# Performance work log

Measured on AMD Instinct MI355X. Metric: run time of the kernel, lower is better.

Reference implementation:

```python
import jax, jax.numpy as jnp
import numpy as np

H = 256   # hidden_dim
S = 16    # d_state
B = 2
N = 8192
LN_EPS = 1e-5


def setup_inputs() -> dict:
    key = jax.random.key(0)
    ks = jax.random.split(key, 12)
    std = 1.0 / np.sqrt(H)
    inp = {
        'x': jax.random.normal(ks[0], (B, N, H), dtype=jnp.float32),
        'in_w': jax.random.normal(ks[1], (2 * H, H), dtype=jnp.float32) * std,
        'in_b': jax.random.normal(ks[2], (2 * H,), dtype=jnp.float32) * std,
        'xp_w': jax.random.normal(ks[3], (2 * S + 1, H), dtype=jnp.float32) * std,
        'xp_b': jax.random.normal(ks[4], (2 * S + 1,), dtype=jnp.float32) * std,
        'dt_w': jax.random.normal(ks[5], (H, 1), dtype=jnp.float32),
        'dt_b': jax.random.normal(ks[6], (H,), dtype=jnp.float32),
        'A_log': jnp.log(jnp.broadcast_to(jnp.arange(1, S + 1, dtype=jnp.float32), (H, S))),
        'D': jnp.ones((H,), dtype=jnp.float32),
        'out_w': jax.random.normal(ks[7], (H, H), dtype=jnp.float32) * std,
        'out_b': jax.random.normal(ks[8], (H,), dtype=jnp.float32) * std,
        'ln_g': jnp.ones((H,), dtype=jnp.float32),
        'ln_b': jnp.zeros((H,), dtype=jnp.float32),
    }
    return inp


def reference(x, in_w, in_b, xp_w, xp_b, dt_w, dt_b, A_log, D, out_w, out_b, ln_g, ln_b):
    # x: (B, N, H). Dropout is identity in eval mode.
    residual = x
    xz = jnp.einsum('bnh,kh->bnk', x, in_w) + in_b            # (B,N,2H)
    x_inner, z = xz[..., :H], xz[..., H:]
    x_dbl = jnp.einsum('bnh,kh->bnk', x_inner, xp_w) + xp_b   # (B,N,2S+1)
    dt_raw = x_dbl[..., :1]
    B_raw = x_dbl[..., 1:S + 1]                               # (B,N,S)
    C_raw = x_dbl[..., S + 1:]                                # (B,N,S)
    dt = jax.nn.softplus(dt_raw * dt_w[:, 0] + dt_b)          # (B,N,H)
    # NOTE: the original computes dA = exp(dt * A) but never uses it; A_log
    # does not affect the output, so we skip materializing dA.
    dB = dt[..., None] * B_raw[:, :, None, :]                 # (B,N,H,S)
    h = jnp.cumsum(x_inner[..., None] * dB, axis=1)           # (B,N,H,S)
    y = jnp.einsum('bnhs,bns->bnh', h, C_raw) + D * x_inner   # (B,N,H)
    y = y * jax.nn.silu(z)
    out = jnp.einsum('bnh,kh->bnk', y, out_w) + out_b
    r = out + residual
    mu = jnp.mean(r, axis=-1, keepdims=True)
    var = jnp.mean((r - mu) ** 2, axis=-1, keepdims=True)
    return ln_g * (r - mu) * jax.lax.rsqrt(var + LN_EPS) + ln_b
```

## Files before the change

### kernel.cpp

```cpp
#include <hip/hip_runtime.h>
#include <hip/hip_bf16.h>


#define HD 256
#define SD 16
#define NSEQ 8192
#define NBATCH 2
#define BN (NBATCH * NSEQ)
#define CHUNK 32
#define NCHUNK (NSEQ / CHUNK)
#define NGRP 16
#define GSZ (NCHUNK / NGRP)
#define LN_EPS 1e-5f

#define NIW (2 * HD * HD)
#define NXP (48 * HD)
#define NOW (HD * HD)

typedef __hip_bfloat16 bf16;
typedef __attribute__((ext_vector_type(8))) short bf16x8;
typedef __attribute__((ext_vector_type(4))) short short4v;
typedef __attribute__((ext_vector_type(4))) float f32x4;

__device__ __forceinline__ float b2f(bf16 v) { return __bfloat162float(v); }
__device__ __forceinline__ short f2bs(float f) {
  union { bf16 b; short s; } u;
  u.b = __float2bfloat16(f);
  return u.s;
}
__device__ __forceinline__ bf16x8 cvt_frag(const float* p) {
  bf16x8 r;
#pragma unroll
  for (int j = 0; j < 8; ++j) r[j] = f2bs(p[j]);
  return r;
}
__device__ __forceinline__ float softplus_f(float a) {
  return (a > 20.f) ? a : __logf(1.f + __expf(a));
}

__global__ __launch_bounds__(256) void k0_weights(
    const float* __restrict__ in_w, const float* __restrict__ xp_w,
    const float* __restrict__ out_w, bf16* __restrict__ wbin,
    bf16* __restrict__ wbxp, bf16* __restrict__ wbout)
{
  const int base = (blockIdx.x * 256 + threadIdx.x) * 4;
  if (base < NIW) {
    f32x4 v = *(const f32x4*)(in_w + base);
    *(short4v*)((short*)wbin + base) =
        short4v{f2bs(v[0]), f2bs(v[1]), f2bs(v[2]), f2bs(v[3])};
  } else if (base < NIW + NXP) {
    const int off = base - NIW;
    short4v s;
    if (off < 33 * HD) {
      f32x4 v = *(const f32x4*)(xp_w + off);
      s = short4v{f2bs(v[0]), f2bs(v[1]), f2bs(v[2]), f2bs(v[3])};
    } else {
      s = short4v{0, 0, 0, 0};
    }
    *(short4v*)((short*)wbxp + off) = s;
  } else if (base < NIW + NXP + NOW) {
    const int off = base - NIW - NXP;
    f32x4 v = *(const f32x4*)(out_w + off);
    *(short4v*)((short*)wbout + off) =
        short4v{f2bs(v[0]), f2bs(v[1]), f2bs(v[2]), f2bs(v[3])};
  }
}

__global__ __launch_bounds__(512) void k1f_in_xp_sum(
    const float* __restrict__ x, const bf16* __restrict__ wbin,
    const float* __restrict__ in_b, const bf16* __restrict__ wbxp,
    const float* __restrict__ xp_b, const float* __restrict__ dt_w,
    const float* __restrict__ dt_b, bf16* __restrict__ xib,
    bf16* __restrict__ zb, float* __restrict__ dbc, float* __restrict__ Mc)
{
  __shared__ float xt[32][260];
  __shared__ float zt[32][260];
  __shared__ float sdbc[32][33];
  const int tid = threadIdx.x;
  const int wave = tid >> 6, lane = tid & 63, q = lane >> 4, l16 = lane & 15;
  const int R0 = blockIdx.x * CHUNK;

  {
    const int row = tid >> 4;
    const int c0 = (tid & 15) * 16;
    const float* src = x + (size_t)(R0 + row) * HD + c0;
#pragma unroll
    for (int j = 0; j < 4; ++j)
      *(f32x4*)&xt[row][c0 + j * 4] = *(const f32x4*)(src + j * 4);
  }
  __syncthreads();

  const int mrow = (wave & 1) * 16;
  const int colBase = (wave >> 1) * 128;
  f32x4 acc[8] = {};
  {
    const bf16* bp = wbin + (size_t)(colBase + l16) * HD + q * 8;
#pragma unroll
    for (int k = 0; k < HD; k += 32) {
      bf16x8 af = cvt_frag(&xt[mrow + l16][k + q * 8]);
#pragma unroll
      for (int t = 0; t < 8; ++t) {
        bf16x8 bfr = *(const bf16x8*)(bp + (size_t)t * 16 * HD + k);
        acc[t] = __builtin_amdgcn_mfma_f32_16x16x32_bf16(af, bfr, acc[t], 0, 0, 0);
      }
    }
  }
  __syncthreads();

  {
    float (*dst)[260] = (wave < 4) ? xt : zt;
    const int cb = (wave < 4) ? colBase : (colBase - 256);
#pragma unroll
    for (int t = 0; t < 8; ++t) {
      const int gcol = colBase + t * 16 + l16;
      const float bias = in_b[gcol];
#pragma unroll
      for (int r = 0; r < 4; ++r)
        dst[mrow + q * 4 + r][cb + t * 16 + l16] = acc[t][r] + bias;
    }
  }
  __syncthreads();

  {
    const int row = tid >> 4;
    const int c0 = (tid & 15) * 16;
    bf16* xd = xib + (size_t)(R0 + row) * HD + c0;
    bf16* zd = zb + (size_t)(R0 + row) * HD + c0;
    *(bf16x8*)xd = cvt_frag(&xt[row][c0]);
    *(bf16x8*)(xd + 8) = cvt_frag(&xt[row][c0 + 8]);
    *(bf16x8*)zd = cvt_frag(&zt[row][c0]);
    *(bf16x8*)(zd + 8) = cvt_frag(&zt[row][c0 + 8]);
  }

  if (wave < 2) {
    f32x4 pacc[3] = {};
    const bf16* pb = wbxp + (size_t)l16 * HD + q * 8;
#pragma unroll
    for (int k = 0; k < HD; k += 32) {
      bf16x8 af = cvt_frag(&xt[wave * 16 + l16][k + q * 8]);
#pragma unroll
      for (int t = 0; t < 3; ++t) {
        bf16x8 bfr = *(const bf16x8*)(pb + (size_t)t * 16 * HD + k);
        pacc[t] = __builtin_amdgcn_mfma_f32_16x16x32_bf16(af, bfr, pacc[t], 0, 0, 0);
      }
    }
#pragma unroll
    for (int t = 0; t < 3; ++t) {
      const int col = t * 16 + l16;
      if (col < 33) {
        const float bias = xp_b[col];
#pragma unroll
        for (int r = 0; r < 4; ++r)
          sdbc[wave * 16 + q * 4 + r][col] = pacc[t][r] + bias;
      }
    }
  }
  __syncthreads();

  {
    const float* sflat = &sdbc[0][0];
    for (int idx = tid; idx < CHUNK * 33; idx += 512)
      dbc[(size_t)R0 * 33 + idx] = sflat[idx];
  }
  {
    const int h = tid & 255;
    const int sh = tid >> 8;
    const float dtw = dt_w[h], dtb = dt_b[h];
    float st[8] = {};
#pragma unroll
    for (int n = 0; n < CHUNK; ++n) {
      const float xv = xt[n][h];
      const float dt = softplus_f(sdbc[n][0] * dtw + dtb);
      const float u = xv * dt;
#pragma unroll
      for (int s = 0; s < 8; ++s) st[s] += u * sdbc[n][1 + sh * 8 + s];
    }
    const int b = R0 >> 13, c = (R0 & (NSEQ - 1)) >> 5;
    float* mp = Mc + ((size_t)(b * NCHUNK + c)) * 4096 + (sh * 8) * HD + h;
#pragma unroll
    for (int s = 0; s < 8; ++s) mp[s * HD] = st[s];
  }
}

__global__ __launch_bounds__(256) void k4a_prefix_local(
    float* __restrict__ Mc, float* __restrict__ Gs)
{
  const int tid = blockIdx.x * 256 + threadIdx.x;
  const int b = tid >> 16;
  const int g = (tid >> 12) & (NGRP - 1);
  const int hs = tid & 4095;
  float run = 0.f;
#pragma unroll
  for (int i = 0; i < GSZ; ++i) {
    const size_t idx = ((size_t)(b * NCHUNK + g * GSZ + i)) * 4096 + hs;
    const float v = Mc[idx];
    Mc[idx] = run;
    run += v;
  }
  Gs[((size_t)(b * NGRP + g)) * 4096 + hs] = run;
}

__global__ __launch_bounds__(256) void k4b_prefix_groups(float* __restrict__ Gs)
{
  const int tid = blockIdx.x * 256 + threadIdx.x;
  const int b = tid >> 12;
  const int hs = tid & 4095;
  float run = 0.f;
#pragma unroll
  for (int g = 0; g < NGRP; ++g) {
    const size_t idx = ((size_t)(b * NGRP + g)) * 4096 + hs;
    const float v = Gs[idx];
    Gs[idx] = run;
    run += v;
  }
}

__global__ __launch_bounds__(512) void k56_scan_out_ln(
    const bf16* __restrict__ xib, const bf16* __restrict__ zb,
    const float* __restrict__ dbc, const float* __restrict__ dt_w,
    const float* __restrict__ dt_b, const float* __restrict__ Dv,
    const float* __restrict__ Mc, const float* __restrict__ Gs,
    const bf16* __restrict__ wbout, const float* __restrict__ out_b,
    const float* __restrict__ x, const float* __restrict__ ln_g,
    const float* __restrict__ ln_b, float* __restrict__ out)
{
  __shared__ float sdbc[CHUNK][33];
  __shared__ float yt[32][260];
  __shared__ float pt[32][260];
  const int tid = threadIdx.x;
  const int wave = tid >> 6, lane = tid & 63, q = lane >> 4, l16 = lane & 15;
  const int R0 = blockIdx.x * CHUNK;
  const int b = R0 >> 13;
  const int cchunk = (R0 & (NSEQ - 1)) >> 5;

  for (int idx = tid; idx < CHUNK * 33; idx += 512) {
    const int n = idx / 33, j = idx - n * 33;
    sdbc[n][j] = dbc[(size_t)(R0 + n) * 33 + j];
  }
  __syncthreads();

  {
    const int h = tid & 255;
    const int sh = tid >> 8;
    const float dtw = dt_w[h], dtb = dt_b[h];
    const float dv = Dv[h];
    float st[8];
    const float* mp = Mc + ((size_t)(b * NCHUNK + cchunk)) * 4096 + sh * 8 * HD + h;
    const float* gp = Gs + ((size_t)(b * NGRP + cchunk / GSZ)) * 4096 + sh * 8 * HD + h;
#pragma unroll
    for (int s = 0; s < 8; ++s) st[s] = mp[s * HD] + gp[s * HD];
    float (*dst)[260] = (sh == 0) ? yt : pt;
    for (int n = 0; n < CHUNK; ++n) {
      const float xv = b2f(xib[(size_t)(R0 + n) * HD + h]);
      const float dt = softplus_f(sdbc[n][0] * dtw + dtb);
      const float u = xv * dt;
      float y = (sh == 0) ? dv * xv : 0.f;
#pragma unroll
      for (int s = 0; s < 8; ++s) {
        st[s] += u * sdbc[n][1 + sh * 8 + s];
        y += st[s] * sdbc[n][17 + sh * 8 + s];
      }
      dst[n][h] = y;
    }
  }
  __syncthreads();

  {
    const int h = tid & 255;
    const int r2 = tid >> 8;
#pragma unroll
    for (int j = 0; j < 16; ++j) {
      const int row = r2 * 16 + j;
      const float zv = b2f(zb[(size_t)(R0 + row) * HD + h]);
      const float sig = 1.f / (1.f + __expf(-zv));
      yt[row][h] = (yt[row][h] + pt[row][h]) * zv * sig;
    }
  }
  __syncthreads();

  const int mrow = (wave & 1) * 16;
  const int colBase = (wave >> 1) * 64;
  f32x4 acc[4] = {};
  {
    const bf16* bp = wbout + (size_t)(colBase + l16) * HD + q * 8;
#pragma unroll
    for (int k = 0; k < HD; k += 32) {
      bf16x8 af = cvt_frag(&yt[mrow + l16][k + q * 8]);
#pragma unroll
      for (int t = 0; t < 4; ++t) {
        bf16x8 bfr = *(const bf16x8*)(bp + (size_t)t * 16 * HD + k);
        acc[t] = __builtin_amdgcn_mfma_f32_16x16x32_bf16(af, bfr, acc[t], 0, 0, 0);
      }
    }
  }
  __syncthreads();

#pragma unroll
  for (int t = 0; t < 4; ++t) {
    const int col = colBase + t * 16 + l16;
    const float bias = out_b[col];
#pragma unroll
    for (int r = 0; r < 4; ++r) {
      const int row = mrow + q * 4 + r;
      pt[row][col] = acc[t][r] + bias + x[(size_t)(R0 + row) * HD + col];
    }
  }
  __syncthreads();

#pragma unroll
  for (int rr = 0; rr < 4; ++rr) {
    const int row = wave * 4 + rr;
    float p = 0.f;
#pragma unroll
    for (int j = 0; j < 4; ++j) p += pt[row][lane + 64 * j];
#pragma unroll
    for (int off = 32; off > 0; off >>= 1) p += __shfl_xor(p, off);
    const float mu = p * (1.f / 256.f);
    float v2 = 0.f;
#pragma unroll
    for (int j = 0; j < 4; ++j) {
      const float d = pt[row][lane + 64 * j] - mu;
      v2 += d * d;
    }
#pragma unroll
    for (int off = 32; off > 0; off >>= 1) v2 += __shfl_xor(v2, off);
    const float rstd = rsqrtf(v2 * (1.f / 256.f) + LN_EPS);
    const size_t base = (size_t)(R0 + row) * HD;
#pragma unroll
    for (int j = 0; j < 4; ++j) {
      const int cc = lane + 64 * j;
      out[base + cc] = ln_g[cc] * (pt[row][cc] - mu) * rstd + ln_b[cc];
    }
  }
}

extern "C" void kernel_launch(void* const* d_in, const int* in_sizes, int n_in,
                              void* d_out, int out_size, void* d_ws, size_t ws_size,
                              hipStream_t stream)
{
  const float* x     = (const float*)d_in[0];
  const float* in_w  = (const float*)d_in[1];
  const float* in_b  = (const float*)d_in[2];
  const float* xp_w  = (const float*)d_in[3];
  const float* xp_b  = (const float*)d_in[4];
  const float* dt_w  = (const float*)d_in[5];
  const float* dt_b  = (const float*)d_in[6];
  const float* Dv    = (const float*)d_in[8];
  const float* out_w = (const float*)d_in[9];
  const float* out_b = (const float*)d_in[10];
  const float* ln_g  = (const float*)d_in[11];
  const float* ln_b  = (const float*)d_in[12];

  char* ws = (char*)d_ws;
  bf16*  xib   = (bf16*)(ws);
  bf16*  zb    = (bf16*)(ws +  8388608);
  float* dbc   = (float*)(ws + 16777216);
  float* Mc    = (float*)(ws + 18939904);
  float* Gs    = (float*)(ws + 27328512);
  bf16*  wbin  = (bf16*)(ws + 27852800);
  bf16*  wbxp  = (bf16*)(ws + 28114944);
  bf16*  wbout = (bf16*)(ws + 28139520);
  float* out   = (float*)d_out;

  hipLaunchKernelGGL(k0_weights, dim3((NIW + NXP + NOW) / 1024), dim3(256),
                     0, stream, in_w, xp_w, out_w, wbin, wbxp, wbout);
  hipLaunchKernelGGL(k1f_in_xp_sum, dim3(BN / CHUNK), dim3(512), 0, stream,
                     x, wbin, in_b, wbxp, xp_b, dt_w, dt_b,
                     xib, zb, dbc, Mc);
  hipLaunchKernelGGL(k4a_prefix_local, dim3(NBATCH * NGRP * 4096 / 256),
                     dim3(256), 0, stream, Mc, Gs);
  hipLaunchKernelGGL(k4b_prefix_groups, dim3(NBATCH * 4096 / 256), dim3(256),
                     0, stream, Gs);
  hipLaunchKernelGGL(k56_scan_out_ln, dim3(BN / CHUNK), dim3(512), 0, stream,
                     xib, zb, dbc, dt_w, dt_b, Dv, Mc, Gs,
                     wbout, out_b, x, ln_g, ln_b, out);
}
```

Before: 169.5 us.

## Split fused in-projection into tiled GEMM plus separate xp/state-sum kernel

Converts x to bf16 in the prep kernel, then runs the in-projection as a standalone 128x128-tiled MFMA GEMM with the weight tile staged in LDS, replacing the per-32-row fused kernel that re-read all in_w from global for every block. The xp projection and chunk-state summation move to a new 256-thread kernel that stages xi and xp weights in LDS. The out-projection in the final kernel is re-tiled so each wave covers both 16-row halves and reuses each weight fragment twice. It adds a kernel launch plus an extra bf16 round-trip of x and xi through global memory.

Measured after the change: 150.3 us. -11.3%, faster.

```diff
diff --git a/kernel.cpp b/kernel.cpp
--- a/kernel.cpp
+++ b/kernel.cpp
@@ -13,6 +13,7 @@
 #define GSZ (NCHUNK / NGRP)
 #define LN_EPS 1e-5f
 
+#define NX  (BN * HD)
 #define NIW (2 * HD * HD)
 #define NXP (48 * HD)
 #define NOW (HD * HD)
@@ -38,18 +39,24 @@
   return (a > 20.f) ? a : __logf(1.f + __expf(a));
 }
 
-__global__ __launch_bounds__(256) void k0_weights(
-    const float* __restrict__ in_w, const float* __restrict__ xp_w,
-    const float* __restrict__ out_w, bf16* __restrict__ wbin,
+__global__ __launch_bounds__(256) void k0_convert(
+    const float* __restrict__ x, const float* __restrict__ in_w,
+    const float* __restrict__ xp_w, const float* __restrict__ out_w,
+    bf16* __restrict__ xb, bf16* __restrict__ wbin,
     bf16* __restrict__ wbxp, bf16* __restrict__ wbout)
 {
   const int base = (blockIdx.x * 256 + threadIdx.x) * 4;
-  if (base < NIW) {
-    f32x4 v = *(const f32x4*)(in_w + base);
-    *(short4v*)((short*)wbin + base) =
+  if (base < NX) {
+    f32x4 v = *(const f32x4*)(x + base);
+    *(short4v*)((short*)xb + base) =
         short4v{f2bs(v[0]), f2bs(v[1]), f2bs(v[2]), f2bs(v[3])};
-  } else if (base < NIW + NXP) {
-    const int off = base - NIW;
+  } else if (base < NX + NIW) {
+    const int off = base - NX;
+    f32x4 v = *(const f32x4*)(in_w + off);
+    *(short4v*)((short*)wbin + off) =
+        short4v{f2bs(v[0]), f2bs(v[1]), f2bs(v[2]), f2bs(v[3])};
+  } else if (base < NX + NIW + NXP) {
+    const int off = base - NX - NIW;
     short4v s;
     if (off < 33 * HD) {
       f32x4 v = *(const f32x4*)(xp_w + off);
@@ -58,89 +65,116 @@
       s = short4v{0, 0, 0, 0};
     }
     *(short4v*)((short*)wbxp + off) = s;
-  } else if (base < NIW + NXP + NOW) {
-    const int off = base - NIW - NXP;
+  } else if (base < NX + NIW + NXP + NOW) {
+    const int off = base - NX - NIW - NXP;
     f32x4 v = *(const f32x4*)(out_w + off);
     *(short4v*)((short*)wbout + off) =
         short4v{f2bs(v[0]), f2bs(v[1]), f2bs(v[2]), f2bs(v[3])};
   }
 }
 
-__global__ __launch_bounds__(512) void k1f_in_xp_sum(
-    const float* __restrict__ x, const bf16* __restrict__ wbin,
-    const float* __restrict__ in_b, const bf16* __restrict__ wbxp,
+__global__ __launch_bounds__(256) void k1_gemm(
+    const bf16* __restrict__ xb, const bf16* __restrict__ wbin,
+    const float* __restrict__ in_b, bf16* __restrict__ xib,
+    bf16* __restrict__ zb)
+{
+  __shared__ __align__(16) char smem[128 * 264 * 2];
+  bf16* Bt = (bf16*)smem;
+  float* Ct = (float*)smem;
+
+  const int tid = threadIdx.x;
+  const int rt = blockIdx.x >> 2, ct = blockIdx.x & 3;
+  const int R0 = rt * 128, C0 = ct * 128;
+  const int wave = tid >> 6, lane = tid & 63, q = lane >> 4, l16 = lane & 15;
+
+#pragma unroll
+  for (int it = 0; it < 16; ++it) {
+    const int f = tid + it * 256;
+    const int row = f >> 5, g = f & 31;
+    bf16x8 v = *(const bf16x8*)(wbin + (size_t)(C0 + row) * HD + g * 8);
+    *(bf16x8*)(Bt + row * 264 + g * 8) = v;
+  }
+  __syncthreads();
+
+  const int rowHalf = (wave & 1) * 64;
+  const int colHalf = (wave >> 1) * 64;
+  f32x4 acc[4][4] = {};
+  const bf16* ap = xb + (size_t)(R0 + rowHalf + l16) * HD + q * 8;
+#pragma unroll
+  for (int k = 0; k < HD; k += 32) {
+    bf16x8 a[4], b[4];
+#pragma unroll
+    for (int i = 0; i < 4; ++i)
+      a[i] = *(const bf16x8*)(ap + (size_t)i * 16 * HD + k);
+#pragma unroll
+    for (int j = 0; j < 4; ++j)
+      b[j] = *(const bf16x8*)(Bt + (colHalf + j * 16 + l16) * 264 + k + q * 8);
+#pragma unroll
+    for (int i = 0; i < 4; ++i)
+#pragma unroll
+      for (int j = 0; j < 4; ++j)
+        acc[i][j] = __builtin_amdgcn_mfma_f32_16x16x32_bf16(a[i], b[j], acc[i][j], 0, 0, 0);
+  }
+  __syncthreads();
+
+#pragma unroll
+  for (int j = 0; j < 4; ++j) {
+    const int col = colHalf + j * 16 + l16;
+    const float bias = in_b[C0 + col];
+#pragma unroll
+    for (int i = 0; i < 4; ++i)
+#pragma unroll
+      for (int r = 0; r < 4; ++r)
+        Ct[(rowHalf + i * 16 + q * 4 + r) * 132 + col] = acc[i][j][r] + bias;
+  }
+  __syncthreads();
+
+  bf16* dst = (C0 < HD) ? xib : zb;
+  const int Cd = (C0 < HD) ? C0 : (C0 - HD);
+#pragma unroll
+  for (int it = 0; it < 8; ++it) {
+    const int f = tid + it * 256;
+    const int row = f >> 4, g = f & 15;
+    bf16x8 v = cvt_frag(Ct + row * 132 + g * 8);
+    *(bf16x8*)(dst + (size_t)(R0 + row) * HD + Cd + g * 8) = v;
+  }
+}
+
+__global__ __launch_bounds__(256) void k2_xp_sum(
+    const bf16* __restrict__ xib, const bf16* __restrict__ wbxp,
     const float* __restrict__ xp_b, const float* __restrict__ dt_w,
-    const float* __restrict__ dt_b, bf16* __restrict__ xib,
-    bf16* __restrict__ zb, float* __restrict__ dbc, float* __restrict__ Mc)
-{
-  __shared__ float xt[32][260];
-  __shared__ float zt[32][260];
+    const float* __restrict__ dt_b, float* __restrict__ dbc,
+    float* __restrict__ Mc)
+{
+  __shared__ bf16 xt[32 * 264];
+  __shared__ bf16 wp[48 * 264];
   __shared__ float sdbc[32][33];
   const int tid = threadIdx.x;
+  const int R0 = blockIdx.x * CHUNK;
   const int wave = tid >> 6, lane = tid & 63, q = lane >> 4, l16 = lane & 15;
-  const int R0 = blockIdx.x * CHUNK;
-
-  {
-    const int row = tid >> 4;
-    const int c0 = (tid & 15) * 16;
-    const float* src = x + (size_t)(R0 + row) * HD + c0;
-#pragma unroll
-    for (int j = 0; j < 4; ++j)
-      *(f32x4*)&xt[row][c0 + j * 4] = *(const f32x4*)(src + j * 4);
-  }
-  __syncthreads();
-
-  const int mrow = (wave & 1) * 16;
-  const int colBase = (wave >> 1) * 128;
-  f32x4 acc[8] = {};
-  {
-    const bf16* bp = wbin + (size_t)(colBase + l16) * HD + q * 8;
-#pragma unroll
-    for (int k = 0; k < HD; k += 32) {
-      bf16x8 af = cvt_frag(&xt[mrow + l16][k + q * 8]);
-#pragma unroll
-      for (int t = 0; t < 8; ++t) {
-        bf16x8 bfr = *(const bf16x8*)(bp + (size_t)t * 16 * HD + k);
-        acc[t] = __builtin_amdgcn_mfma_f32_16x16x32_bf16(af, bfr, acc[t], 0, 0, 0);
-      }
-    }
-  }
-  __syncthreads();
-
-  {
-    float (*dst)[260] = (wave < 4) ? xt : zt;
-    const int cb = (wave < 4) ? colBase : (colBase - 256);
-#pragma unroll
-    for (int t = 0; t < 8; ++t) {
-      const int gcol = colBase + t * 16 + l16;
-      const float bias = in_b[gcol];
-#pragma unroll
-      for (int r = 0; r < 4; ++r)
-        dst[mrow + q * 4 + r][cb + t * 16 + l16] = acc[t][r] + bias;
-    }
-  }
-  __syncthreads();
-
-  {
-    const int row = tid >> 4;
-    const int c0 = (tid & 15) * 16;
-    bf16* xd = xib + (size_t)(R0 + row) * HD + c0;
-    bf16* zd = zb + (size_t)(R0 + row) * HD + c0;
-    *(bf16x8*)xd = cvt_frag(&xt[row][c0]);
-    *(bf16x8*)(xd + 8) = cvt_frag(&xt[row][c0 + 8]);
-    *(bf16x8*)zd = cvt_frag(&zt[row][c0]);
-    *(bf16x8*)(zd + 8) = cvt_frag(&zt[row][c0 + 8]);
-  }
+
+#pragma unroll
+  for (int it = 0; it < 4; ++it) {
+    const int f = tid + it * 256, row = f >> 5, g = f & 31;
+    *(bf16x8*)(xt + row * 264 + g * 8) =
+        *(const bf16x8*)(xib + (size_t)(R0 + row) * HD + g * 8);
+  }
+#pragma unroll
+  for (int it = 0; it < 6; ++it) {
+    const int f = tid + it * 256, row = f >> 5, g = f & 31;
+    *(bf16x8*)(wp + row * 264 + g * 8) =
+        *(const bf16x8*)(wbxp + (size_t)row * HD + g * 8);
+  }
+  __syncthreads();
 
   if (wave < 2) {
     f32x4 pacc[3] = {};
-    const bf16* pb = wbxp + (size_t)l16 * HD + q * 8;
 #pragma unroll
     for (int k = 0; k < HD; k += 32) {
-      bf16x8 af = cvt_frag(&xt[wave * 16 + l16][k + q * 8]);
+      bf16x8 af = *(const bf16x8*)(xt + (wave * 16 + l16) * 264 + k + q * 8);
 #pragma unroll
       for (int t = 0; t < 3; ++t) {
-        bf16x8 bfr = *(const bf16x8*)(pb + (size_t)t * 16 * HD + k);
+        bf16x8 bfr = *(const bf16x8*)(wp + (t * 16 + l16) * 264 + k + q * 8);
         pacc[t] = __builtin_amdgcn_mfma_f32_16x16x32_bf16(af, bfr, pacc[t], 0, 0, 0);
       }
     }
@@ -159,26 +193,25 @@
 
   {
     const float* sflat = &sdbc[0][0];
-    for (int idx = tid; idx < CHUNK * 33; idx += 512)
+    for (int idx = tid; idx < CHUNK * 33; idx += 256)
       dbc[(size_t)R0 * 33 + idx] = sflat[idx];
   }
   {
-    const int h = tid & 255;
-    const int sh = tid >> 8;
+    const int h = tid;
     const float dtw = dt_w[h], dtb = dt_b[h];
-    float st[8] = {};
+    float st[SD] = {};
 #pragma unroll
     for (int n = 0; n < CHUNK; ++n) {
-      const float xv = xt[n][h];
+      const float xv = b2f(xt[n * 264 + h]);
       const float dt = softplus_f(sdbc[n][0] * dtw + dtb);
       const float u = xv * dt;
 #pragma unroll
-      for (int s = 0; s < 8; ++s) st[s] += u * sdbc[n][1 + sh * 8 + s];
+      for (int s = 0; s < SD; ++s) st[s] += u * sdbc[n][1 + s];
     }
     const int b = R0 >> 13, c = (R0 & (NSEQ - 1)) >> 5;
-    float* mp = Mc + ((size_t)(b * NCHUNK + c)) * 4096 + (sh * 8) * HD + h;
-#pragma unroll
-    for (int s = 0; s < 8; ++s) mp[s * HD] = st[s];
+    float* mp = Mc + ((size_t)(b * NCHUNK + c)) * 4096 + h;
+#pragma unroll
+    for (int s = 0; s < SD; ++s) mp[s * HD] = st[s];
   }
 }
 
@@ -278,32 +311,32 @@
   }
   __syncthreads();
 
-  const int mrow = (wave & 1) * 16;
-  const int colBase = (wave >> 1) * 64;
-  f32x4 acc[4] = {};
-  {
-    const bf16* bp = wbout + (size_t)(colBase + l16) * HD + q * 8;
-#pragma unroll
-    for (int k = 0; k < HD; k += 32) {
-      bf16x8 af = cvt_frag(&yt[mrow + l16][k + q * 8]);
-#pragma unroll
-      for (int t = 0; t < 4; ++t) {
-        bf16x8 bfr = *(const bf16x8*)(bp + (size_t)t * 16 * HD + k);
-        acc[t] = __builtin_amdgcn_mfma_f32_16x16x32_bf16(af, bfr, acc[t], 0, 0, 0);
+  const int cw = wave * 32;
+  f32x4 acc[2][2] = {};
+#pragma unroll
+  for (int k = 0; k < HD; k += 32) {
+    bf16x8 a0 = cvt_frag(&yt[l16][k + q * 8]);
+    bf16x8 a1 = cvt_frag(&yt[16 + l16][k + q * 8]);
+#pragma unroll
+    for (int t = 0; t < 2; ++t) {
+      bf16x8 bfr = *(const bf16x8*)(wbout + (size_t)(cw + t * 16 + l16) * HD + k + q * 8);
+      acc[0][t] = __builtin_amdgcn_mfma_f32_16x16x32_bf16(a0, bfr, acc[0][t], 0, 0, 0);
+      acc[1][t] = __builtin_amdgcn_mfma_f32_16x16x32_bf16(a1, bfr, acc[1][t], 0, 0, 0);
+    }
+  }
+  __syncthreads();
+
+#pragma unroll
+  for (int t = 0; t < 2; ++t) {
+    const int col = cw + t * 16 + l16;
+    const float bias = out_b[col];
+#pragma unroll
+    for (int i = 0; i < 2; ++i)
+#pragma unroll
+      for (int r = 0; r < 4; ++r) {
+        const int row = i * 16 + q * 4 + r;
+        pt[row][col] = acc[i][t][r] + bias + x[(size_t)(R0 + row) * HD + col];
       }
-    }
-  }
-  __syncthreads();
-
-#pragma unroll
-  for (int t = 0; t < 4; ++t) {
-    const int col = colBase + t * 16 + l16;
-    const float bias = out_b[col];
-#pragma unroll
-    for (int r = 0; r < 4; ++r) {
-      const int row = mrow + q * 4 + r;
-      pt[row][col] = acc[t][r] + bias + x[(size_t)(R0 + row) * HD + col];
-    }
   }
   __syncthreads();
 
@@ -354,19 +387,21 @@
   char* ws = (char*)d_ws;
   bf16*  xib   = (bf16*)(ws);
   bf16*  zb    = (bf16*)(ws +  8388608);
-  float* dbc   = (float*)(ws + 16777216);
-  float* Mc    = (float*)(ws + 18939904);
-  float* Gs    = (float*)(ws + 27328512);
-  bf16*  wbin  = (bf16*)(ws + 27852800);
-  bf16*  wbxp  = (bf16*)(ws + 28114944);
-  bf16*  wbout = (bf16*)(ws + 28139520);
+  bf16*  xb    = (bf16*)(ws + 16777216);
+  float* dbc   = (float*)(ws + 25165824);
+  float* Mc    = (float*)(ws + 27328512);
+  float* Gs    = (float*)(ws + 35717120);
+  bf16*  wbin  = (bf16*)(ws + 36241408);
+  bf16*  wbxp  = (bf16*)(ws + 36503552);
+  bf16*  wbout = (bf16*)(ws + 36528128);
   float* out   = (float*)d_out;
 
-  hipLaunchKernelGGL(k0_weights, dim3((NIW + NXP + NOW) / 1024), dim3(256),
-                     0, stream, in_w, xp_w, out_w, wbin, wbxp, wbout);
-  hipLaunchKernelGGL(k1f_in_xp_sum, dim3(BN / CHUNK), dim3(512), 0, stream,
-                     x, wbin, in_b, wbxp, xp_b, dt_w, dt_b,
-                     xib, zb, dbc, Mc);
+  hipLaunchKernelGGL(k0_convert, dim3((NX + NIW + NXP + NOW) / 1024), dim3(256),
+                     0, stream, x, in_w, xp_w, out_w, xb, wbin, wbxp, wbout);
+  hipLaunchKernelGGL(k1_gemm, dim3(512), dim3(256), 0, stream,
+                     xb, wbin, in_b, xib, zb);
+  hipLaunchKernelGGL(k2_xp_sum, dim3(BN / CHUNK), dim3(256), 0, stream,
+                     xib, wbxp, xp_b, dt_w, dt_b, dbc, Mc);
   hipLaunchKernelGGL(k4a_prefix_local, dim3(NBATCH * NGRP * 4096 / 256),
                      dim3(256), 0, stream, Mc, Gs);
   hipLaunchKernelGGL(k4b_prefix_groups, dim3(NBATCH * 4096 / 256), dim3(256),
```
